# Optimization experiments

Hardware: AMD Instinct MI355X
Metric: run time of the kernel (lower is better)

The kernel has to match this reference:

```python
import jax, jax.numpy as jnp
import numpy as np

N_NODES = 50000
N_EDGES = 800000
IN_DIM = 256
HID = 32
HEADS = 8
OUT_DIM = 16


def gat_layer(x, src, dst, W, att_s, att_d, bias, concat):
    """PyG-style GATConv (eval mode, add_self_loops already applied to src/dst)."""
    N = x.shape[0]
    H, C = att_s.shape
    h = (x @ W).reshape(N, H, C)                       # [N, H, C]
    a_s = jnp.sum(h * att_s, axis=-1)                  # [N, H]
    a_d = jnp.sum(h * att_d, axis=-1)                  # [N, H]
    alpha = jax.nn.leaky_relu(a_s[src] + a_d[dst], negative_slope=0.2)  # [E, H]
    # segment softmax over edges grouped by destination node
    m = jax.ops.segment_max(alpha, dst, num_segments=N)                 # [N, H]
    e = jnp.exp(alpha - m[dst])
    s = jax.ops.segment_sum(e, dst, num_segments=N)
    coef = e / (s[dst] + 1e-16)                                         # [E, H]
    out = jax.ops.segment_sum(coef[:, :, None] * h[src], dst, num_segments=N)  # [N, H, C]
    out = out.reshape(N, H * C) if concat else out.mean(axis=1)
    return out + bias


def setup_inputs() -> dict:
    key = jax.random.key(0)
    ks = jax.random.split(key, 10)
    x = jax.random.normal(ks[0], (N_NODES, IN_DIM), dtype=jnp.float32)
    edge_index = jax.random.randint(ks[1], (2, N_EDGES), 0, N_NODES, dtype=jnp.int32)
    sc = 0.05
    W1 = jax.random.normal(ks[2], (IN_DIM, HEADS * HID), dtype=jnp.float32) * sc
    att_src1 = jax.random.normal(ks[3], (HEADS, HID), dtype=jnp.float32) * sc
    att_dst1 = jax.random.normal(ks[4], (HEADS, HID), dtype=jnp.float32) * sc
    b1 = jnp.zeros((HEADS * HID,), dtype=jnp.float32)
    W2 = jax.random.normal(ks[5], (HEADS * HID, OUT_DIM), dtype=jnp.float32) * sc
    att_src2 = jax.random.normal(ks[6], (1, OUT_DIM), dtype=jnp.float32) * sc
    att_dst2 = jax.random.normal(ks[7], (1, OUT_DIM), dtype=jnp.float32) * sc
    b2 = jnp.zeros((OUT_DIM,), dtype=jnp.float32)
    return {"x": x, "edge_index": edge_index,
            "W1": W1, "att_src1": att_src1, "att_dst1": att_dst1, "b1": b1,
            "W2": W2, "att_src2": att_src2, "att_dst2": att_dst2, "b2": b2}


def reference(x, edge_index, W1, att_src1, att_dst1, b1, W2, att_src2, att_dst2, b2):
    N = x.shape[0]
    loops = jnp.arange(N, dtype=edge_index.dtype)      # GATConv add_self_loops=True
    src = jnp.concatenate([edge_index[0], loops])
    dst = jnp.concatenate([edge_index[1], loops])
    h = jax.nn.elu(gat_layer(x, src, dst, W1, att_src1, att_dst1, b1, concat=True))
    out = gat_layer(h, src, dst, W2, att_src2, att_dst2, b2, concat=False)
    return out
```

## Files before the change

### kernel.cpp

```cpp
#include <hip/hip_runtime.h>

#define N_NODES 50000
#define N_EDGES 800000
#define E_TOT   (N_EDGES + N_NODES)
#define IN_DIM  256
#define HID     32
#define HEADS   8
#define D1      256
#define OUT_DIM 16

#define SCAN_CHUNK 1024
#define SCAN_NB ((N_NODES + SCAN_CHUNK - 1) / SCAN_CHUNK)
#define CNT8_NB ((E_TOT + 2047) / 2048)
#define G1_NB   ((D1 / 128) * ((N_NODES + 127) / 128))

typedef __attribute__((ext_vector_type(8))) short bf16x8;
typedef __attribute__((ext_vector_type(4))) float f32x4;
typedef __attribute__((ext_vector_type(4))) _Float16 half4;
typedef __attribute__((ext_vector_type(8))) _Float16 half8;

__device__ __forceinline__ unsigned short f2bf(float f) {
  unsigned u = __float_as_uint(f);
  return (unsigned short)((u + 0x7FFFu + ((u >> 16) & 1u)) >> 16);
}
__device__ __forceinline__ float bf2f(unsigned short b) {
  return __uint_as_float(((unsigned)b) << 16);
}
__device__ __forceinline__ float lrelu(float a) { return (a > 0.f) ? a : 0.2f * a; }

__global__ void prep_w(const float* __restrict__ W, unsigned short* __restrict__ Wth,
                       unsigned short* __restrict__ Wtl) {
  int t = blockIdx.x * blockDim.x + threadIdx.x;
  if (t >= IN_DIM * D1) return;
  int n = t >> 8, k = t & 255;
  float v = W[k * D1 + n];
  unsigned short h = f2bf(v);
  Wth[n * IN_DIM + k] = h;
  Wtl[n * IN_DIM + k] = f2bf(v - bf2f(h));
}

__global__ __launch_bounds__(256) void gemm1_count(
    const float* __restrict__ x,
    const unsigned short* __restrict__ Bth_g, const unsigned short* __restrict__ Btl_g,
    const float* __restrict__ att_s, const float* __restrict__ att_d,
    _Float16* __restrict__ C, float* __restrict__ as_, float* __restrict__ ad_,
    const int* __restrict__ edst, int* __restrict__ deg, int* __restrict__ rank) {
  const int bid = blockIdx.x;
  if (bid < CNT8_NB) {
    const int eb = bid * 2048 + threadIdx.x;
    #pragma unroll
    for (int u = 0; u < 8; u++) {
      int e = eb + u * 256;
      if (e < E_TOT) {
        int d = (e < N_EDGES) ? edst[e] : (e - N_EDGES);
        rank[e] = atomicAdd(&deg[d], 1);
      }
    }
    return;
  }
  __shared__ short Ah[128][40], Al[128][40];
  __shared__ short Bh[128][40], Bl[128][40];
  const int gb = bid - CNT8_NB;
  const int bm = (gb >> 1) * 128, bn = (gb & 1) * 128;
  const int tid = threadIdx.x;
  const int wave = tid >> 6, lane = tid & 63;
  const int l15 = lane & 15, l4 = lane >> 4;
  f32x4 acc[8][2] = {};
  const int sr2 = tid >> 1, sc2 = (tid & 1) * 16;
  const bf16x8 zv = {0, 0, 0, 0, 0, 0, 0, 0};
  for (int k0 = 0; k0 < IN_DIM; k0 += 32) {
    int grow = bm + sr2;
    if (grow < N_NODES) {
      const float4* xp = (const float4*)&x[(size_t)grow * IN_DIM + k0 + sc2];
      #pragma unroll
      for (int j = 0; j < 4; j++) {
        float4 v = xp[j];
        ushort4 hh, ll;
        hh.x = f2bf(v.x); ll.x = f2bf(v.x - bf2f(hh.x));
        hh.y = f2bf(v.y); ll.y = f2bf(v.y - bf2f(hh.y));
        hh.z = f2bf(v.z); ll.z = f2bf(v.z - bf2f(hh.z));
        hh.w = f2bf(v.w); ll.w = f2bf(v.w - bf2f(hh.w));
        *(ushort4*)&Ah[sr2][sc2 + j * 4] = hh;
        *(ushort4*)&Al[sr2][sc2 + j * 4] = ll;
      }
    } else {
      *(bf16x8*)&Ah[sr2][sc2] = zv;
      *(bf16x8*)&Ah[sr2][sc2 + 8] = zv;
      *(bf16x8*)&Al[sr2][sc2] = zv;
      *(bf16x8*)&Al[sr2][sc2 + 8] = zv;
    }
    {
      const bf16x8* sH = (const bf16x8*)&Bth_g[(size_t)(bn + sr2) * IN_DIM + k0 + sc2];
      const bf16x8* sL = (const bf16x8*)&Btl_g[(size_t)(bn + sr2) * IN_DIM + k0 + sc2];
      *(bf16x8*)&Bh[sr2][sc2] = sH[0];
      *(bf16x8*)&Bh[sr2][sc2 + 8] = sH[1];
      *(bf16x8*)&Bl[sr2][sc2] = sL[0];
      *(bf16x8*)&Bl[sr2][sc2 + 8] = sL[1];
    }
    __syncthreads();
    bf16x8 bh0 = *(bf16x8*)&Bh[wave * 32 + l15][l4 * 8];
    bf16x8 bl0 = *(bf16x8*)&Bl[wave * 32 + l15][l4 * 8];
    bf16x8 bh1 = *(bf16x8*)&Bh[wave * 32 + 16 + l15][l4 * 8];
    bf16x8 bl1 = *(bf16x8*)&Bl[wave * 32 + 16 + l15][l4 * 8];
    #pragma unroll
    for (int i = 0; i < 8; i++) {
      bf16x8 ah = *(bf16x8*)&Ah[i * 16 + l15][l4 * 8];
      bf16x8 al = *(bf16x8*)&Al[i * 16 + l15][l4 * 8];
      acc[i][0] = __builtin_amdgcn_mfma_f32_16x16x32_bf16(ah, bh0, acc[i][0], 0, 0, 0);
      acc[i][0] = __builtin_amdgcn_mfma_f32_16x16x32_bf16(ah, bl0, acc[i][0], 0, 0, 0);
      acc[i][0] = __builtin_amdgcn_mfma_f32_16x16x32_bf16(al, bh0, acc[i][0], 0, 0, 0);
      acc[i][1] = __builtin_amdgcn_mfma_f32_16x16x32_bf16(ah, bh1, acc[i][1], 0, 0, 0);
      acc[i][1] = __builtin_amdgcn_mfma_f32_16x16x32_bf16(ah, bl1, acc[i][1], 0, 0, 0);
      acc[i][1] = __builtin_amdgcn_mfma_f32_16x16x32_bf16(al, bh1, acc[i][1], 0, 0, 0);
    }
    __syncthreads();
  }
  const int head = (bn >> 5) + wave;
  const float sA0 = att_s[head * HID + l15];
  const float sA1 = att_s[head * HID + 16 + l15];
  const float dA0 = att_d[head * HID + l15];
  const float dA1 = att_d[head * HID + 16 + l15];
  #pragma unroll
  for (int i = 0; i < 8; i++) {
    #pragma unroll
    for (int cf = 0; cf < 2; cf++) {
      const int ccol = bn + wave * 32 + cf * 16 + l15;
      #pragma unroll
      for (int r = 0; r < 4; r++) {
        int crow = bm + i * 16 + l4 * 4 + r;
        if (crow < N_NODES) C[(size_t)crow * D1 + ccol] = (_Float16)acc[i][cf][r];
      }
    }
    float ps[4], pd[4];
    #pragma unroll
    for (int r = 0; r < 4; r++) {
      ps[r] = acc[i][0][r] * sA0 + acc[i][1][r] * sA1;
      pd[r] = acc[i][0][r] * dA0 + acc[i][1][r] * dA1;
    }
    #pragma unroll
    for (int m = 1; m < 16; m <<= 1) {
      #pragma unroll
      for (int r = 0; r < 4; r++) {
        ps[r] += __shfl_xor(ps[r], m);
        pd[r] += __shfl_xor(pd[r], m);
      }
    }
    if (l15 == 0) {
      #pragma unroll
      for (int r = 0; r < 4; r++) {
        int crow = bm + i * 16 + l4 * 4 + r;
        if (crow < N_NODES) {
          as_[crow * HEADS + head] = ps[r];
          ad_[crow * HEADS + head] = pd[r];
        }
      }
    }
  }
}

__global__ __launch_bounds__(256) void scan_partial(const int* __restrict__ deg,
                                                    int* __restrict__ offs,
                                                    int* __restrict__ part) {
  __shared__ int ts[256];
  const int tid = threadIdx.x;
  const int idx = blockIdx.x * SCAN_CHUNK + tid * 4;
  int4 v = {0, 0, 0, 0};
  if (idx + 3 < N_NODES) {
    v = *(const int4*)(deg + idx);
  } else {
    if (idx + 0 < N_NODES) v.x = deg[idx + 0];
    if (idx + 1 < N_NODES) v.y = deg[idx + 1];
    if (idx + 2 < N_NODES) v.z = deg[idx + 2];
  }
  ts[tid] = v.x + v.y + v.z + v.w;
  __syncthreads();
  for (int st = 1; st < 256; st <<= 1) {
    int t = (tid >= st) ? ts[tid - st] : 0;
    __syncthreads();
    ts[tid] += t;
    __syncthreads();
  }
  if (tid == 255) part[blockIdx.x] = ts[255];
  int o0 = (tid == 0) ? 0 : ts[tid - 1];
  int4 o;
  o.x = o0; o.y = o0 + v.x; o.z = o.y + v.y; o.w = o.z + v.z;
  if (idx + 3 < N_NODES) {
    *(int4*)(offs + idx) = o;
  } else {
    if (idx + 0 < N_NODES) offs[idx + 0] = o.x;
    if (idx + 1 < N_NODES) offs[idx + 1] = o.y;
    if (idx + 2 < N_NODES) offs[idx + 2] = o.z;
  }
}

__global__ __launch_bounds__(256) void scan_apply(int* __restrict__ offs,
                                                  const int* __restrict__ part) {
  __shared__ int sp[SCAN_NB];
  const int tid = threadIdx.x;
  if (tid < SCAN_NB) sp[tid] = part[tid];
  __syncthreads();
  if (tid == 0) {
    int run = 0;
    #pragma unroll 1
    for (int b = 0; b < SCAN_NB; b++) { int v = sp[b]; sp[b] = run; run += v; }
  }
  __syncthreads();
  int t = blockIdx.x * 256 + tid;
  if (t < N_NODES) offs[t] += sp[t >> 10];
}

__global__ void scatter_edges(const int* __restrict__ esrc, const int* __restrict__ edst,
                              const int* __restrict__ offs, const int* __restrict__ rank,
                              int* __restrict__ srcs) {
  int e = blockIdx.x * blockDim.x + threadIdx.x;
  if (e >= E_TOT) return;
  int s = (e < N_EDGES) ? esrc[e] : (e - N_EDGES);
  int d = (e < N_EDGES) ? edst[e] : (e - N_EDGES);
  srcs[offs[d] + rank[e]] = s;
}

__global__ __launch_bounds__(256) void node_aggr1(
    const int* __restrict__ offs, const int* __restrict__ deg,
    const int* __restrict__ srcs,
    const float* __restrict__ as_, const float* __restrict__ ad_,
    const _Float16* __restrict__ h, const float* __restrict__ bias,
    _Float16* __restrict__ out) {
  const int n = blockIdx.x * 4 + (threadIdx.x >> 6);
  const int lane = threadIdx.x & 63;
  const int base = offs[n], dg = deg[n];
  const int hd = lane >> 3;
  const float adn = ad_[n * HEADS + hd];
  const unsigned c0 = lane * 4;
  float4 acc = {0.f, 0.f, 0.f, 0.f};
  float se = 0.f;
  int e = 0;
  for (; e + 8 <= dg; e += 8) {
    int s[8];
    #pragma unroll
    for (int u = 0; u < 8; u++) s[u] = __builtin_amdgcn_readfirstlane(srcs[base + e + u]);
    half4 hv[8];
    #pragma unroll
    for (int u = 0; u < 8; u++) hv[u] = *(const half4*)(h + ((unsigned)s[u] * D1 + c0));
    float ex[8];
    #pragma unroll
    for (int u = 0; u < 8; u++) ex[u] = __expf(lrelu(as_[(unsigned)s[u] * HEADS + hd] + adn));
    #pragma unroll
    for (int u = 0; u < 8; u++) {
      se += ex[u];
      acc.x += ex[u] * (float)hv[u].x; acc.y += ex[u] * (float)hv[u].y;
      acc.z += ex[u] * (float)hv[u].z; acc.w += ex[u] * (float)hv[u].w;
    }
  }
  for (; e + 4 <= dg; e += 4) {
    int s[4];
    #pragma unroll
    for (int u = 0; u < 4; u++) s[u] = __builtin_amdgcn_readfirstlane(srcs[base + e + u]);
    half4 hv[4];
    #pragma unroll
    for (int u = 0; u < 4; u++) hv[u] = *(const half4*)(h + ((unsigned)s[u] * D1 + c0));
    float ex[4];
    #pragma unroll
    for (int u = 0; u < 4; u++) ex[u] = __expf(lrelu(as_[(unsigned)s[u] * HEADS + hd] + adn));
    #pragma unroll
    for (int u = 0; u < 4; u++) {
      se += ex[u];
      acc.x += ex[u] * (float)hv[u].x; acc.y += ex[u] * (float)hv[u].y;
      acc.z += ex[u] * (float)hv[u].z; acc.w += ex[u] * (float)hv[u].w;
    }
  }
  for (; e < dg; e++) {
    int s = __builtin_amdgcn_readfirstlane(srcs[base + e]);
    float ex = __expf(lrelu(as_[(unsigned)s * HEADS + hd] + adn));
    half4 hv = *(const half4*)(h + ((unsigned)s * D1 + c0));
    se += ex;
    acc.x += ex * (float)hv.x; acc.y += ex * (float)hv.y;
    acc.z += ex * (float)hv.z; acc.w += ex * (float)hv.w;
  }
  const float inv = 1.f / (se + 1e-16f);
  float4 bv = *(const float4*)(bias + c0);
  float4 v;
  v.x = acc.x * inv + bv.x; v.y = acc.y * inv + bv.y;
  v.z = acc.z * inv + bv.z; v.w = acc.w * inv + bv.w;
  v.x = (v.x > 0.f) ? v.x : expm1f(v.x);
  v.y = (v.y > 0.f) ? v.y : expm1f(v.y);
  v.z = (v.z > 0.f) ? v.z : expm1f(v.z);
  v.w = (v.w > 0.f) ? v.w : expm1f(v.w);
  half4 ov;
  ov.x = (_Float16)v.x; ov.y = (_Float16)v.y; ov.z = (_Float16)v.z; ov.w = (_Float16)v.w;
  *(half4*)(out + ((unsigned)n * D1 + c0)) = ov;
}

__global__ __launch_bounds__(256) void gemm2_attn2(
    const _Float16* __restrict__ A, const float* __restrict__ B,
    const float* __restrict__ att_s, const float* __restrict__ att_d,
    _Float16* __restrict__ C, float* __restrict__ as_, float* __restrict__ ad_) {
  __shared__ float Bs[D1 * OUT_DIM];
  const int tid = threadIdx.x;
  #pragma unroll
  for (int i = 0; i < D1 * OUT_DIM / 4 / 256; i++)
    ((float4*)Bs)[tid + i * 256] = ((const float4*)B)[tid + i * 256];
  __syncthreads();
  const int t = blockIdx.x * 256 + tid;
  const int n = t >> 4, c = t & 15;
  const _Float16* arow = A + (size_t)n * D1;
  float acc = 0.f;
  #pragma unroll
  for (int k0 = 0; k0 < D1; k0 += 8) {
    half8 av = *(const half8*)&arow[k0];
    #pragma unroll
    for (int j = 0; j < 8; j++) acc += (float)av[j] * Bs[(k0 + j) * OUT_DIM + c];
  }
  C[t] = (_Float16)acc;
  float ps = acc * att_s[c], pd = acc * att_d[c];
  #pragma unroll
  for (int mS = 1; mS < 16; mS <<= 1) {
    ps += __shfl_xor(ps, mS);
    pd += __shfl_xor(pd, mS);
  }
  if (c == 0) { as_[n] = ps; ad_[n] = pd; }
}

__global__ __launch_bounds__(256) void node_aggr2(
    const int* __restrict__ offs, const int* __restrict__ deg,
    const int* __restrict__ srcs,
    const float* __restrict__ as_, const float* __restrict__ ad_,
    const _Float16* __restrict__ g, const float* __restrict__ bias,
    float* __restrict__ out) {
  const int n = blockIdx.x * 4 + (threadIdx.x >> 6);
  const int lane = threadIdx.x & 63;
  const int base = offs[n], dg = deg[n];
  const float adn = ad_[n];
  const int c = lane & 15, grp = lane >> 4;
  float acc = 0.f, se = 0.f;
  int e = grp;
  for (; e + 8 <= dg + grp; e += 8) {
    unsigned s0 = srcs[base + e], s1 = srcs[base + e + 4];
    float e0 = __expf(lrelu(as_[s0] + adn));
    float e1 = __expf(lrelu(as_[s1] + adn));
    float g0 = (float)g[s0 * OUT_DIM + c], g1 = (float)g[s1 * OUT_DIM + c];
    se += e0 + e1;
    acc += e0 * g0 + e1 * g1;
  }
  for (; e < dg; e += 4) {
    unsigned s = srcs[base + e];
    float ex = __expf(lrelu(as_[s] + adn));
    se += ex;
    acc += ex * (float)g[s * OUT_DIM + c];
  }
  acc += __shfl_xor(acc, 16); se += __shfl_xor(se, 16);
  acc += __shfl_xor(acc, 32); se += __shfl_xor(se, 32);
  if (lane < OUT_DIM) out[n * OUT_DIM + c] = acc / (se + 1e-16f) + bias[c];
}

extern "C" void kernel_launch(void* const* d_in, const int* in_sizes, int n_in,
                              void* d_out, int out_size, void* d_ws, size_t ws_size,
                              hipStream_t stream) {
  const float* x      = (const float*)d_in[0];
  const int*   ei     = (const int*)d_in[1];
  const float* W1     = (const float*)d_in[2];
  const float* att_s1 = (const float*)d_in[3];
  const float* att_d1 = (const float*)d_in[4];
  const float* b1     = (const float*)d_in[5];
  const float* W2     = (const float*)d_in[6];
  const float* att_s2 = (const float*)d_in[7];
  const float* att_d2 = (const float*)d_in[8];
  const float* b2     = (const float*)d_in[9];
  float* out = (float*)d_out;
  const int* esrc = ei;
  const int* edst = ei + N_EDGES;

  char* w = (char*)d_ws;
  _Float16* h1f = (_Float16*)w; w += (size_t)N_NODES * D1 * 2;
  _Float16* h2  = (_Float16*)w; w += (size_t)N_NODES * D1 * 2;
  unsigned short* W1t_hi = (unsigned short*)w;  w += (size_t)IN_DIM * D1 * 2;
  unsigned short* W1t_lo = (unsigned short*)w;  w += (size_t)IN_DIM * D1 * 2;
  float* as1 = (float*)w;       w += (size_t)N_NODES * HEADS * 4;
  float* ad1 = (float*)w;       w += (size_t)N_NODES * HEADS * 4;
  _Float16* g2 = (_Float16*)w;  w += (size_t)N_NODES * OUT_DIM * 2;
  float* as2 = (float*)w;       w += (size_t)N_NODES * 4;
  float* ad2 = (float*)w;       w += (size_t)N_NODES * 4;
  int* deg   = (int*)w;         w += (size_t)N_NODES * 4;
  int* offs  = (int*)w;         w += (size_t)N_NODES * 4;
  int* part  = (int*)w;         w += (size_t)64 * 4;
  int* rank  = (int*)w;         w += (size_t)E_TOT * 4;
  int* srcs  = (int*)w;         w += (size_t)E_TOT * 4;

  hipMemsetAsync(deg, 0, (size_t)N_NODES * 4, stream);

  prep_w<<<IN_DIM * D1 / 256, 256, 0, stream>>>(W1, W1t_hi, W1t_lo);

  gemm1_count<<<CNT8_NB + G1_NB, 256, 0, stream>>>(
      x, W1t_hi, W1t_lo, att_s1, att_d1, h1f, as1, ad1, edst, deg, rank);

  scan_partial<<<SCAN_NB, 256, 0, stream>>>(deg, offs, part);
  scan_apply<<<(N_NODES + 255) / 256, 256, 0, stream>>>(offs, part);
  scatter_edges<<<(E_TOT + 255) / 256, 256, 0, stream>>>(esrc, edst, offs, rank, srcs);

  node_aggr1<<<N_NODES / 4, 256, 0, stream>>>(offs, deg, srcs, as1, ad1, h1f, b1, h2);

  gemm2_attn2<<<N_NODES * OUT_DIM / 256, 256, 0, stream>>>(
      h2, W2, att_s2, att_d2, g2, as2, ad2);

  node_aggr2<<<N_NODES / 4, 256, 0, stream>>>(offs, deg, srcs, as2, ad2, g2, b2, out);
}
```

Before: 207.2 us.

## Split degree counters into four sub-counters and place self-loops at segment end

The degree counting atomics now go into four sub-counters per node, chosen by edge index modulo four, so fewer atomics contend on the same address. The scan produces per-node sub-prefix offsets (pre4) used when scattering edges. Self-loops are no longer counted with atomics: each node's self-loop goes into the last slot of its CSR segment, written during scan_apply. The trade-off is a fourfold larger counter array and memset, plus an extra int4 gather per edge during the scatter.

```diff
diff --git a/kernel.cpp b/kernel.cpp
--- a/kernel.cpp
+++ b/kernel.cpp
@@ -9,9 +9,8 @@
 #define D1      256
 #define OUT_DIM 16
 
-#define SCAN_CHUNK 1024
-#define SCAN_NB ((N_NODES + SCAN_CHUNK - 1) / SCAN_CHUNK)
-#define CNT8_NB ((E_TOT + 2047) / 2048)
+#define SCAN_NB ((N_NODES + 255) / 256)
+#define CNT8_NB ((N_EDGES + 2047) / 2048)
 #define G1_NB   ((D1 / 128) * ((N_NODES + 127) / 128))
 
 typedef __attribute__((ext_vector_type(8))) short bf16x8;
@@ -44,16 +43,16 @@
     const unsigned short* __restrict__ Bth_g, const unsigned short* __restrict__ Btl_g,
     const float* __restrict__ att_s, const float* __restrict__ att_d,
     _Float16* __restrict__ C, float* __restrict__ as_, float* __restrict__ ad_,
-    const int* __restrict__ edst, int* __restrict__ deg, int* __restrict__ rank) {
+    const int* __restrict__ edst, int* __restrict__ deg4, int* __restrict__ rank) {
   const int bid = blockIdx.x;
   if (bid < CNT8_NB) {
     const int eb = bid * 2048 + threadIdx.x;
     #pragma unroll
     for (int u = 0; u < 8; u++) {
       int e = eb + u * 256;
-      if (e < E_TOT) {
-        int d = (e < N_EDGES) ? edst[e] : (e - N_EDGES);
-        rank[e] = atomicAdd(&deg[d], 1);
+      if (e < N_EDGES) {
+        int d = edst[e];
+        rank[e] = atomicAdd(&deg4[(d << 2) + (e & 3)], 1);
       }
     }
     return;
@@ -158,21 +157,21 @@
   }
 }
 
-__global__ __launch_bounds__(256) void scan_partial(const int* __restrict__ deg,
+__global__ __launch_bounds__(256) void scan_partial(const int* __restrict__ deg4,
+                                                    int4* __restrict__ pre4,
+                                                    int* __restrict__ deg,
                                                     int* __restrict__ offs,
                                                     int* __restrict__ part) {
   __shared__ int ts[256];
   const int tid = threadIdx.x;
-  const int idx = blockIdx.x * SCAN_CHUNK + tid * 4;
+  const int n = blockIdx.x * 256 + tid;
   int4 v = {0, 0, 0, 0};
-  if (idx + 3 < N_NODES) {
-    v = *(const int4*)(deg + idx);
-  } else {
-    if (idx + 0 < N_NODES) v.x = deg[idx + 0];
-    if (idx + 1 < N_NODES) v.y = deg[idx + 1];
-    if (idx + 2 < N_NODES) v.z = deg[idx + 2];
-  }
-  ts[tid] = v.x + v.y + v.z + v.w;
+  if (n < N_NODES) v = *(const int4*)(deg4 + n * 4);
+  int4 p;
+  p.x = 0; p.y = v.x; p.z = v.x + v.y; p.w = v.x + v.y + v.z;
+  const int tot = p.w + v.w + 1;
+  if (n < N_NODES) { pre4[n] = p; deg[n] = tot; }
+  ts[tid] = (n < N_NODES) ? tot : 0;
   __syncthreads();
   for (int st = 1; st < 256; st <<= 1) {
     int t = (tid >= st) ? ts[tid - st] : 0;
@@ -181,20 +180,13 @@
     __syncthreads();
   }
   if (tid == 255) part[blockIdx.x] = ts[255];
-  int o0 = (tid == 0) ? 0 : ts[tid - 1];
-  int4 o;
-  o.x = o0; o.y = o0 + v.x; o.z = o.y + v.y; o.w = o.z + v.z;
-  if (idx + 3 < N_NODES) {
-    *(int4*)(offs + idx) = o;
-  } else {
-    if (idx + 0 < N_NODES) offs[idx + 0] = o.x;
-    if (idx + 1 < N_NODES) offs[idx + 1] = o.y;
-    if (idx + 2 < N_NODES) offs[idx + 2] = o.z;
-  }
+  if (n < N_NODES) offs[n] = ts[tid] - tot;
 }
 
 __global__ __launch_bounds__(256) void scan_apply(int* __restrict__ offs,
-                                                  const int* __restrict__ part) {
+                                                  const int* __restrict__ part,
+                                                  const int* __restrict__ deg,
+                                                  int* __restrict__ srcs) {
   __shared__ int sp[SCAN_NB];
   const int tid = threadIdx.x;
   if (tid < SCAN_NB) sp[tid] = part[tid];
@@ -205,18 +197,24 @@
     for (int b = 0; b < SCAN_NB; b++) { int v = sp[b]; sp[b] = run; run += v; }
   }
   __syncthreads();
-  int t = blockIdx.x * 256 + tid;
-  if (t < N_NODES) offs[t] += sp[t >> 10];
+  int n = blockIdx.x * 256 + tid;
+  if (n < N_NODES) {
+    int o = offs[n] + sp[n >> 8];
+    offs[n] = o;
+    srcs[o + deg[n] - 1] = n;
+  }
 }
 
 __global__ void scatter_edges(const int* __restrict__ esrc, const int* __restrict__ edst,
-                              const int* __restrict__ offs, const int* __restrict__ rank,
-                              int* __restrict__ srcs) {
+                              const int* __restrict__ offs, const int4* __restrict__ pre4,
+                              const int* __restrict__ rank, int* __restrict__ srcs) {
   int e = blockIdx.x * blockDim.x + threadIdx.x;
-  if (e >= E_TOT) return;
-  int s = (e < N_EDGES) ? esrc[e] : (e - N_EDGES);
-  int d = (e < N_EDGES) ? edst[e] : (e - N_EDGES);
-  srcs[offs[d] + rank[e]] = s;
+  if (e >= N_EDGES) return;
+  int s = esrc[e], d = edst[e];
+  int4 p = pre4[d];
+  int j = e & 3;
+  int pj = (j == 0) ? p.x : (j == 1) ? p.y : (j == 2) ? p.z : p.w;
+  srcs[offs[d] + pj + rank[e]] = s;
 }
 
 __global__ __launch_bounds__(256) void node_aggr1(
@@ -379,22 +377,24 @@
   _Float16* g2 = (_Float16*)w;  w += (size_t)N_NODES * OUT_DIM * 2;
   float* as2 = (float*)w;       w += (size_t)N_NODES * 4;
   float* ad2 = (float*)w;       w += (size_t)N_NODES * 4;
+  int* deg4  = (int*)w;         w += (size_t)N_NODES * 16;
+  int4* pre4 = (int4*)w;        w += (size_t)N_NODES * 16;
   int* deg   = (int*)w;         w += (size_t)N_NODES * 4;
   int* offs  = (int*)w;         w += (size_t)N_NODES * 4;
-  int* part  = (int*)w;         w += (size_t)64 * 4;
-  int* rank  = (int*)w;         w += (size_t)E_TOT * 4;
+  int* part  = (int*)w;         w += (size_t)256 * 4;
+  int* rank  = (int*)w;         w += (size_t)N_EDGES * 4;
   int* srcs  = (int*)w;         w += (size_t)E_TOT * 4;
 
-  hipMemsetAsync(deg, 0, (size_t)N_NODES * 4, stream);
+  hipMemsetAsync(deg4, 0, (size_t)N_NODES * 16, stream);
 
   prep_w<<<IN_DIM * D1 / 256, 256, 0, stream>>>(W1, W1t_hi, W1t_lo);
 
   gemm1_count<<<CNT8_NB + G1_NB, 256, 0, stream>>>(
-      x, W1t_hi, W1t_lo, att_s1, att_d1, h1f, as1, ad1, edst, deg, rank);
-
-  scan_partial<<<SCAN_NB, 256, 0, stream>>>(deg, offs, part);
-  scan_apply<<<(N_NODES + 255) / 256, 256, 0, stream>>>(offs, part);
-  scatter_edges<<<(E_TOT + 255) / 256, 256, 0, stream>>>(esrc, edst, offs, rank, srcs);
+      x, W1t_hi, W1t_lo, att_s1, att_d1, h1f, as1, ad1, edst, deg4, rank);
+
+  scan_partial<<<SCAN_NB, 256, 0, stream>>>(deg4, pre4, deg, offs, part);
+  scan_apply<<<SCAN_NB, 256, 0, stream>>>(offs, part, deg, srcs);
+  scatter_edges<<<(N_EDGES + 255) / 256, 256, 0, stream>>>(esrc, edst, offs, pre4, rank, srcs);
 
   node_aggr1<<<N_NODES / 4, 256, 0, stream>>>(offs, deg, srcs, as1, ad1, h1f, b1, h2);
 
```

Measured after the change: 209.1 us. About the same (+0.9%).
